# Optimization experiments

Measured on AMD Instinct MI355X. Metric: run time of the kernel, lower is better.

The kernel has to match this reference:

```python
import jax, jax.numpy as jnp
import numpy as np

DIM = 128
N = 16          # num_nodes
B = 8           # batch size
H = 4096        # MLP hidden width
SLOPE = 0.01    # LeakyReLU default negative slope
PI_ITERS = 50   # fixed-iteration power iteration (max_error=1e-5 regime)


def setup_inputs() -> dict:
    key = jax.random.key(0)
    ks = jax.random.split(key, 12)
    w = lambda k, shape: jax.random.normal(k, shape, jnp.float32) * 0.02
    return {
        "nodes_embeddings": jax.random.normal(ks[0], (B, N, DIM), jnp.float32),
        "graphs_embeddings": jax.random.normal(ks[1], (B, DIM), jnp.float32),
        "Ts": jax.random.uniform(ks[2], (B, N, N), jnp.float32),
        "W1": w(ks[3], (2 * DIM, H)), "b1": jnp.zeros((H,), jnp.float32),
        "W2": w(ks[4], (H, H)),       "b2": jnp.zeros((H,), jnp.float32),
        "W3": w(ks[5], (H, H)),       "b3": jnp.zeros((H,), jnp.float32),
        "W4": w(ks[6], (H, N * N)),   "b4": jnp.zeros((N * N,), jnp.float32),
    }


def _mlp(x, W1, b1, W2, b2, W3, b3, W4, b4):
    # Linear -> LeakyReLU -> (Dropout=eval identity), x3, then Linear -> LeakyReLU -> Sigmoid
    h = jax.nn.leaky_relu(x @ W1 + b1, SLOPE)
    h = jax.nn.leaky_relu(h @ W2 + b2, SLOPE)
    h = jax.nn.leaky_relu(h @ W3 + b3, SLOPE)
    return jax.nn.sigmoid(jax.nn.leaky_relu(h @ W4 + b4, SLOPE))


def _power_iteration(A):
    # A: (..., n, n), entries > 0 (sigmoid outputs) -> dominant (Perron) eigenvector.
    v0 = jnp.ones(A.shape[:-1], A.dtype)
    def step(v, _):
        w = jnp.einsum('...ij,...j->...i', A, v)
        v = w / jnp.linalg.norm(w, axis=-1, keepdims=True)
        return v, None
    v, _ = jax.lax.scan(step, v0, None, length=PI_ITERS)
    return v


def reference(nodes_embeddings, graphs_embeddings, Ts, W1, b1, W2, b2, W3, b3, W4, b4):
    Bn, Nn, D = nodes_embeddings.shape
    P = Nn * Nn
    pair = jnp.arange(P)
    s_ids = pair // Nn  # outer loop index s
    t_ids = pair % Nn   # inner loop index t

    embT = jnp.transpose(nodes_embeddings, (1, 0, 2))      # (N, B, D)
    s_all = embT[s_ids]                                    # (P, B, D)
    t_all = embT[t_ids]                                    # (P, B, D)
    # Faithful to torch.stack([s, t]).view(batch, 2*dim): a flat reinterpretation,
    # NOT a per-row concat. stack axis=1 -> (P, 2, B, D) then reshape -> (P, B, 2D).
    x = jnp.stack([s_all, t_all], axis=1).reshape(P, Bn, 2 * D)

    pol = _mlp(x.reshape(P * Bn, 2 * D), W1, b1, W2, b2, W3, b3, W4, b4)
    pol = pol.reshape(P, Bn, Nn, Nn)                       # predecessor prob matrices

    vec = _power_iteration(pol)                            # (P, B, N)
    v_src = vec[pair, :, s_ids]                            # (P, B) eigenvector[src]
    T_pair = jnp.transpose(Ts.reshape(Bn, P), (1, 0))      # (P, B), pair order s*N+t

    contrib = vec / v_src[:, :, None] * T_pair[:, :, None]  # (P, B, N)
    return jnp.sum(contrib, axis=0)                         # (B, N) == Cs
```

## Files before the change

### kernel.cpp

```cpp
#include <hip/hip_runtime.h>

typedef unsigned short u16;
typedef unsigned int u32;
typedef __attribute__((ext_vector_type(8))) short short8;
typedef __attribute__((ext_vector_type(4))) float f32x4;

__device__ __forceinline__ u16 f2bf(float f) {
    unsigned u = __float_as_uint(f);
    return (u16)((u + 0x7FFFu + ((u >> 16) & 1u)) >> 16);
}
__device__ __forceinline__ u32 pack2(float a, float b) {
    return ((u32)f2bf(b) << 16) | (u32)f2bf(a);
}

#define ROR1 0x121
#define ROR2 0x122
#define ROR4 0x124
#define ROR8 0x128
template<int C> __device__ __forceinline__ float dppf(float x) {
    int i = __float_as_int(x);
    return __int_as_float(__builtin_amdgcn_update_dpp(i, i, C, 0xF, 0xF, false));
}
template<int C> __device__ __forceinline__ int dppi(int x) {
    return __builtin_amdgcn_update_dpp(x, x, C, 0xF, 0xF, false);
}

__device__ __forceinline__ void stage_w(const float* __restrict__ W, int N,
                                        int krow0, int c0, int wv, int lane,
                                        u16 (*Wlds)[136])
{
    int cb = wv * 8;
    const float* s0 = W + (size_t)(krow0 + 2 * lane) * N + c0 + cb;
    float4 r0a = ((const float4*)s0)[0];
    float4 r0b = ((const float4*)s0)[1];
    const float* s1 = s0 + N;
    float4 r1a = ((const float4*)s1)[0];
    float4 r1b = ((const float4*)s1)[1];
    u32* wb = (u32*)&Wlds[0][0];
    wb[(cb + 0) * 68 + lane] = pack2(r0a.x, r1a.x);
    wb[(cb + 1) * 68 + lane] = pack2(r0a.y, r1a.y);
    wb[(cb + 2) * 68 + lane] = pack2(r0a.z, r1a.z);
    wb[(cb + 3) * 68 + lane] = pack2(r0a.w, r1a.w);
    wb[(cb + 4) * 68 + lane] = pack2(r0b.x, r1b.x);
    wb[(cb + 5) * 68 + lane] = pack2(r0b.y, r1b.y);
    wb[(cb + 6) * 68 + lane] = pack2(r0b.z, r1b.z);
    wb[(cb + 7) * 68 + lane] = pack2(r0b.w, r1b.w);
}

__global__ __launch_bounds__(256) void k_gemm(
    const u16* __restrict__ A,
    const float* __restrict__ W,
    float* __restrict__ Cp,
    int K, int N, int kchunk)
{
    __shared__ __align__(16) u16 Alds[64][136];
    __shared__ __align__(16) u16 Wlds[32][136];
    int tid = threadIdx.x;
    int wv = tid >> 6, lane = tid & 63, c = lane & 15, g = lane >> 4;
    int c0 = blockIdx.x * 32;
    int k0 = blockIdx.y * kchunk;
    f32x4 acc0 = {0.f,0.f,0.f,0.f}, acc1 = {0.f,0.f,0.f,0.f};

    for (int kc = 0; kc < kchunk; kc += 128) {
        {
            int row = tid >> 2, seg = tid & 3;
            const uint4* src = (const uint4*)(A + (size_t)row * K + k0 + kc + seg * 32);
            uint4* dst = (uint4*)&Alds[row][seg * 32];
            dst[0] = src[0]; dst[1] = src[1]; dst[2] = src[2]; dst[3] = src[3];
        }
        stage_w(W, N, k0 + kc, c0, wv, lane, Wlds);
        __syncthreads();
        #pragma unroll
        for (int ks = 0; ks < 4; ++ks) {
            int kk = ks * 32 + g * 8;
            short8 a8 = *(const short8*)&Alds[wv * 16 + c][kk];
            short8 b0 = *(const short8*)&Wlds[c][kk];
            short8 b1 = *(const short8*)&Wlds[16 + c][kk];
            acc0 = __builtin_amdgcn_mfma_f32_16x16x32_bf16(a8, b0, acc0, 0, 0, 0);
            acc1 = __builtin_amdgcn_mfma_f32_16x16x32_bf16(a8, b1, acc1, 0, 0, 0);
        }
        __syncthreads();
    }
    float* out = Cp + (size_t)blockIdx.y * 64 * N;
    int rbase = wv * 16 + g * 4;
    #pragma unroll
    for (int rr = 0; rr < 4; ++rr) {
        out[(size_t)(rbase + rr) * N + c0 + c]      = acc0[rr];
        out[(size_t)(rbase + rr) * N + c0 + 16 + c] = acc1[rr];
    }
}

__global__ __launch_bounds__(256) void k_gemm_l1(
    const float* __restrict__ emb,
    const float* __restrict__ W,
    float* __restrict__ Cp)
{
    __shared__ __align__(16) u16 Alds[64][136];
    __shared__ __align__(16) u16 Wlds[32][136];
    int tid = threadIdx.x;
    int wv = tid >> 6, lane = tid & 63, c = lane & 15, g = lane >> 4;
    int c0 = blockIdx.x * 32;
    int half = blockIdx.y;
    f32x4 acc0 = {0.f,0.f,0.f,0.f}, acc1 = {0.f,0.f,0.f,0.f};

    {
        int row = tid >> 2, seg = tid & 3;
        int b = 2 * (row & 3) + half, nd = row >> 2;
        const float4* src = (const float4*)(emb + (b * 16 + nd) * 128 + seg * 32);
        u32* dst = (u32*)&Alds[row][seg * 32];
        #pragma unroll
        for (int t = 0; t < 8; ++t) {
            float4 f = src[t];
            dst[2 * t]     = pack2(f.x, f.y);
            dst[2 * t + 1] = pack2(f.z, f.w);
        }
    }
    stage_w(W, 4096, half * 128, c0, wv, lane, Wlds);
    __syncthreads();
    #pragma unroll
    for (int ks = 0; ks < 4; ++ks) {
        int kk = ks * 32 + g * 8;
        short8 a8 = *(const short8*)&Alds[wv * 16 + c][kk];
        short8 b0 = *(const short8*)&Wlds[c][kk];
        short8 b1 = *(const short8*)&Wlds[16 + c][kk];
        acc0 = __builtin_amdgcn_mfma_f32_16x16x32_bf16(a8, b0, acc0, 0, 0, 0);
        acc1 = __builtin_amdgcn_mfma_f32_16x16x32_bf16(a8, b1, acc1, 0, 0, 0);
    }
    float* out = Cp + (size_t)half * 64 * 4096;
    int rbase = wv * 16 + g * 4;
    #pragma unroll
    for (int rr = 0; rr < 4; ++rr) {
        out[(size_t)(rbase + rr) * 4096 + c0 + c]      = acc0[rr];
        out[(size_t)(rbase + rr) * 4096 + c0 + 16 + c] = acc1[rr];
    }
}

__global__ void k_reduce(const float* __restrict__ Cp, const float* __restrict__ bias,
                         u16* __restrict__ Hb, float* __restrict__ Pf,
                         int N, int ksplit, int mode)
{
    int idx = blockIdx.x * 256 + threadIdx.x;
    int col = idx & (N - 1);
    float s = bias[col];
    for (int k = 0; k < ksplit; ++k) s += Cp[(size_t)k * 64 * N + idx];
    float a = (s >= 0.f) ? s : 0.01f * s;
    if (mode == 0) Hb[idx] = f2bf(a);
    else           Pf[idx] = 1.0f / (1.0f + __expf(-a));
}

__global__ __launch_bounds__(1024) void k_power_out(
    const float* __restrict__ pol,
    const float* __restrict__ Ts,
    float* __restrict__ out)
{
    __shared__ float pol_lds[16384];
    __shared__ float w_lds[64][16];
    __shared__ float Ts_lds[2048];
    __shared__ float Cmat[8][16];

    int tid = threadIdx.x;
    int m = tid >> 4, r = tid & 15;

    {
        const float4* p4 = (const float4*)(pol + tid * 16);
        float4* q4 = (float4*)&pol_lds[tid * 16];
        q4[0] = p4[0]; q4[1] = p4[1]; q4[2] = p4[2]; q4[3] = p4[3];
    }
    Ts_lds[tid] = Ts[tid];
    Ts_lds[tid + 1024] = Ts[tid + 1024];
    __syncthreads();

    float Mr[8], Ms[8];
    {
        int mb = m * 256 + r * 16;
        int idx = r;
        #pragma unroll
        for (int k = 0; k < 8; ++k) { Mr[k] = pol_lds[mb + idx]; idx = dppi<ROR1>(idx); }
        #pragma unroll
        for (int k = 0; k < 8; ++k) { Ms[k] = pol_lds[mb + idx]; idx = dppi<ROR1>(idx); }
    }

    float v = 1.0f;
    #pragma unroll 1
    for (int it = 0; it < 50; ++it) {
        float va = v, vb = dppf<ROR8>(v);
        float w = 0.f, w2 = 0.f;
        #pragma unroll
        for (int k = 0; k < 8; ++k) {
            w  = fmaf(Mr[k], va, w);
            w2 = fmaf(Ms[k], vb, w2);
            if (k < 7) { va = dppf<ROR1>(va); vb = dppf<ROR1>(vb); }
        }
        w += w2;
        if ((it & 7) == 7) {
            float s = w;
            s += dppf<ROR8>(s); s += dppf<ROR4>(s);
            s += dppf<ROR2>(s); s += dppf<ROR1>(s);
            w *= 1.0f / s;
        }
        v = w;
    }
    w_lds[m][r] = v;
    __syncthreads();

    if (tid < 128) {
        int b = tid >> 4, x = tid & 15;
        float s = 0.f;
        if (b < 4) {
            const float* row = &Ts_lds[(b * 16 + x) * 16];
            #pragma unroll
            for (int t = 0; t < 16; ++t) s += row[t];
        } else {
            int j = b - 4;
            #pragma unroll
            for (int si = 0; si < 16; ++si)
                s += Ts_lds[(b * 16 + si) * 16 + x] / w_lds[x * 4 + j][si];
        }
        Cmat[b][x] = s;
    }
    __syncthreads();

    if (tid < 128) {
        int b = tid >> 4, n = tid & 15;
        float o = 0.f;
        if (b < 4) {
            #pragma unroll
            for (int si = 0; si < 16; ++si) {
                const float* wr = w_lds[si * 4 + b];
                o += wr[n] / wr[si] * Cmat[b][si];
            }
        } else {
            int j = b - 4;
            #pragma unroll
            for (int t = 0; t < 16; ++t)
                o += w_lds[t * 4 + j][n] * Cmat[b][t];
        }
        out[b * 16 + n] = o;
    }
}

extern "C" void kernel_launch(void* const* d_in, const int* in_sizes, int n_in,
                              void* d_out, int out_size, void* d_ws, size_t ws_size,
                              hipStream_t stream)
{
    const float* emb = (const float*)d_in[0];
    const float* Ts  = (const float*)d_in[2];
    const float* W1  = (const float*)d_in[3];  const float* b1 = (const float*)d_in[4];
    const float* W2  = (const float*)d_in[5];  const float* b2 = (const float*)d_in[6];
    const float* W3  = (const float*)d_in[7];  const float* b3 = (const float*)d_in[8];
    const float* W4  = (const float*)d_in[9];  const float* b4 = (const float*)d_in[10];
    float* outp = (float*)d_out;

    char* ws = (char*)d_ws;
    u16*   Ha  = (u16*)(ws + 0);
    u16*   Hb  = (u16*)(ws + 524288);
    float* pol = (float*)(ws + 1048576);
    float* Cp  = (float*)(ws + 1114112);

    int KS = 16;
    while (KS > 2 && (size_t)1114112 + (size_t)KS * 1048576 > ws_size) KS >>= 1;
    int kchunk = 4096 / KS;

    k_gemm_l1<<<dim3(128, 2), 256, 0, stream>>>(emb, W1, Cp);
    k_reduce<<<1024, 256, 0, stream>>>(Cp, b1, Ha, nullptr, 4096, 2, 0);

    k_gemm<<<dim3(128, KS), 256, 0, stream>>>(Ha, W2, Cp, 4096, 4096, kchunk);
    k_reduce<<<1024, 256, 0, stream>>>(Cp, b2, Hb, nullptr, 4096, KS, 0);

    k_gemm<<<dim3(128, KS), 256, 0, stream>>>(Hb, W3, Cp, 4096, 4096, kchunk);
    k_reduce<<<1024, 256, 0, stream>>>(Cp, b3, Ha, nullptr, 4096, KS, 0);

    k_gemm<<<dim3(8, 32), 256, 0, stream>>>(Ha, W4, Cp, 4096, 256, 128);
    k_reduce<<<64, 256, 0, stream>>>(Cp, b4, nullptr, pol, 256, 32, 1);

    k_power_out<<<1, 1024, 0, stream>>>(pol, Ts, outp);

    (void)in_sizes; (void)n_in; (void)out_size; (void)ws_size;
}
```

Measured before the change: 94.26 us.

## Fuse whole MLP and power iteration into one cooperative persistent kernel

Replaces the chain of nine kernel launches with one cooperative kernel of 1024 blocks that uses grid-wide syncs between stages: the layer-1 GEMM, split-K GEMMs, reductions, the final sigmoid, a power iteration spread over four blocks, and the output combine. The GEMM inner loop also gains register prefetch of the next A/W chunk, and the split-K factor for the large layers drops from 16 to 8. The aim is to remove launch gaps and stage tails. The cost is grid.sync overhead and the need for all blocks to be co-resident, with a fallback to the separate launches if that is not possible.

```diff
diff --git a/kernel.cpp b/kernel.cpp
--- a/kernel.cpp
+++ b/kernel.cpp
@@ -1,4 +1,7 @@
 #include <hip/hip_runtime.h>
+#include <hip/hip_cooperative_groups.h>
+
+namespace cg = cooperative_groups;
 
 typedef unsigned short u16;
 typedef unsigned int u32;
@@ -25,51 +28,50 @@
     return __builtin_amdgcn_update_dpp(x, x, C, 0xF, 0xF, false);
 }
 
-__device__ __forceinline__ void stage_w(const float* __restrict__ W, int N,
-                                        int krow0, int c0, int wv, int lane,
-                                        u16 (*Wlds)[136])
-{
+__device__ __forceinline__ void gemm_slice(
+    const u16* __restrict__ A, const float* __restrict__ W,
+    float* __restrict__ outC, int K, int N, int c0, int k0, int nchunk,
+    u16 (*Alds)[136], u16 (*Wlds)[136], int tid)
+{
+    int wv = tid >> 6, lane = tid & 63, c = lane & 15, g = lane >> 4;
+    int arow = tid >> 2, aseg = tid & 3;
     int cb = wv * 8;
-    const float* s0 = W + (size_t)(krow0 + 2 * lane) * N + c0 + cb;
-    float4 r0a = ((const float4*)s0)[0];
-    float4 r0b = ((const float4*)s0)[1];
-    const float* s1 = s0 + N;
-    float4 r1a = ((const float4*)s1)[0];
-    float4 r1b = ((const float4*)s1)[1];
-    u32* wb = (u32*)&Wlds[0][0];
-    wb[(cb + 0) * 68 + lane] = pack2(r0a.x, r1a.x);
-    wb[(cb + 1) * 68 + lane] = pack2(r0a.y, r1a.y);
-    wb[(cb + 2) * 68 + lane] = pack2(r0a.z, r1a.z);
-    wb[(cb + 3) * 68 + lane] = pack2(r0a.w, r1a.w);
-    wb[(cb + 4) * 68 + lane] = pack2(r0b.x, r1b.x);
-    wb[(cb + 5) * 68 + lane] = pack2(r0b.y, r1b.y);
-    wb[(cb + 6) * 68 + lane] = pack2(r0b.z, r1b.z);
-    wb[(cb + 7) * 68 + lane] = pack2(r0b.w, r1b.w);
-}
-
-__global__ __launch_bounds__(256) void k_gemm(
-    const u16* __restrict__ A,
-    const float* __restrict__ W,
-    float* __restrict__ Cp,
-    int K, int N, int kchunk)
-{
-    __shared__ __align__(16) u16 Alds[64][136];
-    __shared__ __align__(16) u16 Wlds[32][136];
-    int tid = threadIdx.x;
-    int wv = tid >> 6, lane = tid & 63, c = lane & 15, g = lane >> 4;
-    int c0 = blockIdx.x * 32;
-    int k0 = blockIdx.y * kchunk;
     f32x4 acc0 = {0.f,0.f,0.f,0.f}, acc1 = {0.f,0.f,0.f,0.f};
 
-    for (int kc = 0; kc < kchunk; kc += 128) {
+    uint4 ar0, ar1, ar2, ar3;
+    float4 w0, w1, w2, w3;
+    {
+        const uint4* asrc = (const uint4*)(A + (size_t)arow * K + k0 + aseg * 32);
+        ar0 = asrc[0]; ar1 = asrc[1]; ar2 = asrc[2]; ar3 = asrc[3];
+        const float* s0 = W + (size_t)(k0 + 2 * lane) * N + c0 + cb;
+        w0 = ((const float4*)s0)[0]; w1 = ((const float4*)s0)[1];
+        const float* s1 = s0 + N;
+        w2 = ((const float4*)s1)[0]; w3 = ((const float4*)s1)[1];
+    }
+    for (int ch = 0; ch < nchunk; ++ch) {
         {
-            int row = tid >> 2, seg = tid & 3;
-            const uint4* src = (const uint4*)(A + (size_t)row * K + k0 + kc + seg * 32);
-            uint4* dst = (uint4*)&Alds[row][seg * 32];
-            dst[0] = src[0]; dst[1] = src[1]; dst[2] = src[2]; dst[3] = src[3];
-        }
-        stage_w(W, N, k0 + kc, c0, wv, lane, Wlds);
-        __syncthreads();
+            uint4* dst = (uint4*)&Alds[arow][aseg * 32];
+            dst[0] = ar0; dst[1] = ar1; dst[2] = ar2; dst[3] = ar3;
+            u32* wb = (u32*)&Wlds[0][0];
+            wb[(cb + 0) * 68 + lane] = pack2(w0.x, w2.x);
+            wb[(cb + 1) * 68 + lane] = pack2(w0.y, w2.y);
+            wb[(cb + 2) * 68 + lane] = pack2(w0.z, w2.z);
+            wb[(cb + 3) * 68 + lane] = pack2(w0.w, w2.w);
+            wb[(cb + 4) * 68 + lane] = pack2(w1.x, w3.x);
+            wb[(cb + 5) * 68 + lane] = pack2(w1.y, w3.y);
+            wb[(cb + 6) * 68 + lane] = pack2(w1.z, w3.z);
+            wb[(cb + 7) * 68 + lane] = pack2(w1.w, w3.w);
+        }
+        __syncthreads();
+        if (ch + 1 < nchunk) {
+            int kn = k0 + (ch + 1) * 128;
+            const uint4* asrc = (const uint4*)(A + (size_t)arow * K + kn + aseg * 32);
+            ar0 = asrc[0]; ar1 = asrc[1]; ar2 = asrc[2]; ar3 = asrc[3];
+            const float* s0 = W + (size_t)(kn + 2 * lane) * N + c0 + cb;
+            w0 = ((const float4*)s0)[0]; w1 = ((const float4*)s0)[1];
+            const float* s1 = s0 + N;
+            w2 = ((const float4*)s1)[0]; w3 = ((const float4*)s1)[1];
+        }
         #pragma unroll
         for (int ks = 0; ks < 4; ++ks) {
             int kk = ks * 32 + g * 8;
@@ -81,18 +83,241 @@
         }
         __syncthreads();
     }
-    float* out = Cp + (size_t)blockIdx.y * 64 * N;
     int rbase = wv * 16 + g * 4;
     #pragma unroll
     for (int rr = 0; rr < 4; ++rr) {
-        out[(size_t)(rbase + rr) * N + c0 + c]      = acc0[rr];
-        out[(size_t)(rbase + rr) * N + c0 + 16 + c] = acc1[rr];
-    }
+        outC[(size_t)(rbase + rr) * N + c0 + c]      = acc0[rr];
+        outC[(size_t)(rbase + rr) * N + c0 + 16 + c] = acc1[rr];
+    }
+}
+
+struct MegaP {
+    const float *emb, *Ts, *W1, *b1, *W2, *b2, *W3, *b3, *W4, *b4;
+    float* out;
+    u16 *Ha, *Hb;
+    float *Cp, *wvec;
+};
+
+__global__ __launch_bounds__(256) void mega(MegaP p)
+{
+    __shared__ __align__(16) u16 Alds[64][136];
+    __shared__ __align__(16) u16 Wlds[32][136];
+    cg::grid_group grid = cg::this_grid();
+    int bid = blockIdx.x, tid = threadIdx.x;
+    int wv = tid >> 6, lane = tid & 63, c = lane & 15, g = lane >> 4;
+
+    if (bid < 256) {
+        int c0 = (bid & 127) * 32, half = bid >> 7;
+        {
+            int row = tid >> 2, seg = tid & 3;
+            int b = 2 * (row & 3) + half, nd = row >> 2;
+            const float4* src = (const float4*)(p.emb + (b * 16 + nd) * 128 + seg * 32);
+            u32* dst = (u32*)&Alds[row][seg * 32];
+            #pragma unroll
+            for (int t = 0; t < 8; ++t) {
+                float4 f = src[t];
+                dst[2 * t]     = pack2(f.x, f.y);
+                dst[2 * t + 1] = pack2(f.z, f.w);
+            }
+        }
+        {
+            int cb = wv * 8;
+            const float* s0 = p.W1 + (size_t)(half * 128 + 2 * lane) * 4096 + c0 + cb;
+            float4 r0a = ((const float4*)s0)[0], r0b = ((const float4*)s0)[1];
+            const float* s1 = s0 + 4096;
+            float4 r1a = ((const float4*)s1)[0], r1b = ((const float4*)s1)[1];
+            u32* wb = (u32*)&Wlds[0][0];
+            wb[(cb + 0) * 68 + lane] = pack2(r0a.x, r1a.x);
+            wb[(cb + 1) * 68 + lane] = pack2(r0a.y, r1a.y);
+            wb[(cb + 2) * 68 + lane] = pack2(r0a.z, r1a.z);
+            wb[(cb + 3) * 68 + lane] = pack2(r0a.w, r1a.w);
+            wb[(cb + 4) * 68 + lane] = pack2(r0b.x, r1b.x);
+            wb[(cb + 5) * 68 + lane] = pack2(r0b.y, r1b.y);
+            wb[(cb + 6) * 68 + lane] = pack2(r0b.z, r1b.z);
+            wb[(cb + 7) * 68 + lane] = pack2(r0b.w, r1b.w);
+        }
+        __syncthreads();
+        f32x4 acc0 = {0.f,0.f,0.f,0.f}, acc1 = {0.f,0.f,0.f,0.f};
+        #pragma unroll
+        for (int ks = 0; ks < 4; ++ks) {
+            int kk = ks * 32 + g * 8;
+            short8 a8 = *(const short8*)&Alds[wv * 16 + c][kk];
+            short8 b0 = *(const short8*)&Wlds[c][kk];
+            short8 b1 = *(const short8*)&Wlds[16 + c][kk];
+            acc0 = __builtin_amdgcn_mfma_f32_16x16x32_bf16(a8, b0, acc0, 0, 0, 0);
+            acc1 = __builtin_amdgcn_mfma_f32_16x16x32_bf16(a8, b1, acc1, 0, 0, 0);
+        }
+        float* out = p.Cp + (size_t)half * 262144;
+        int rbase = wv * 16 + g * 4;
+        #pragma unroll
+        for (int rr = 0; rr < 4; ++rr) {
+            out[(size_t)(rbase + rr) * 4096 + c0 + c]      = acc0[rr];
+            out[(size_t)(rbase + rr) * 4096 + c0 + 16 + c] = acc1[rr];
+        }
+        __syncthreads();
+    }
+    grid.sync();
+
+    {
+        int idx = bid * 256 + tid;
+        int col = idx & 4095;
+        float s = p.b1[col] + p.Cp[idx] + p.Cp[262144 + idx];
+        s = (s >= 0.f) ? s : 0.01f * s;
+        p.Ha[idx] = f2bf(s);
+    }
+    grid.sync();
+
+    gemm_slice(p.Ha, p.W2, p.Cp + (size_t)(bid >> 7) * 262144,
+               4096, 4096, (bid & 127) * 32, (bid >> 7) * 512, 4, Alds, Wlds, tid);
+    grid.sync();
+
+    {
+        int idx = bid * 256 + tid;
+        int col = idx & 4095;
+        float s = p.b2[col];
+        #pragma unroll
+        for (int k = 0; k < 8; ++k) s += p.Cp[(size_t)k * 262144 + idx];
+        s = (s >= 0.f) ? s : 0.01f * s;
+        p.Hb[idx] = f2bf(s);
+    }
+    grid.sync();
+
+    gemm_slice(p.Hb, p.W3, p.Cp + (size_t)(bid >> 7) * 262144,
+               4096, 4096, (bid & 127) * 32, (bid >> 7) * 512, 4, Alds, Wlds, tid);
+    grid.sync();
+
+    {
+        int idx = bid * 256 + tid;
+        int col = idx & 4095;
+        float s = p.b3[col];
+        #pragma unroll
+        for (int k = 0; k < 8; ++k) s += p.Cp[(size_t)k * 262144 + idx];
+        s = (s >= 0.f) ? s : 0.01f * s;
+        p.Ha[idx] = f2bf(s);
+    }
+    grid.sync();
+
+    if (bid < 256)
+        gemm_slice(p.Ha, p.W4, p.Cp + (size_t)(bid >> 3) * 16384,
+                   4096, 256, (bid & 7) * 32, (bid >> 3) * 128, 1, Alds, Wlds, tid);
+    grid.sync();
+
+    if (bid < 4) {
+        float* pol_lds = (float*)&Alds[0][0];
+        {
+            int lr = tid >> 4;
+            int gr = (bid << 4) + lr;
+            int cb4 = (tid & 15) << 4;
+            float accv[16];
+            #pragma unroll
+            for (int j = 0; j < 16; ++j) accv[j] = p.b4[cb4 + j];
+            for (int k = 0; k < 32; ++k) {
+                const float4* q = (const float4*)(p.Cp + (size_t)k * 16384 + gr * 256 + cb4);
+                #pragma unroll
+                for (int j = 0; j < 4; ++j) {
+                    float4 v = q[j];
+                    accv[4*j+0] += v.x; accv[4*j+1] += v.y;
+                    accv[4*j+2] += v.z; accv[4*j+3] += v.w;
+                }
+            }
+            #pragma unroll
+            for (int j = 0; j < 16; ++j) {
+                float a = accv[j];
+                a = (a >= 0.f) ? a : 0.01f * a;
+                pol_lds[lr * 256 + cb4 + j] = 1.0f / (1.0f + __expf(-a));
+            }
+        }
+        __syncthreads();
+        float Mr[8], Ms[8];
+        {
+            int mb = (tid >> 4) * 256 + (tid & 15) * 16;
+            int idx = tid & 15;
+            #pragma unroll
+            for (int k = 0; k < 8; ++k) { Mr[k] = pol_lds[mb + idx]; idx = dppi<ROR1>(idx); }
+            #pragma unroll
+            for (int k = 0; k < 8; ++k) { Ms[k] = pol_lds[mb + idx]; idx = dppi<ROR1>(idx); }
+        }
+        float v = 1.0f;
+        #pragma unroll 1
+        for (int it = 0; it < 50; ++it) {
+            float va = v, vb = dppf<ROR8>(v);
+            float w = 0.f, w2 = 0.f;
+            #pragma unroll
+            for (int k = 0; k < 8; ++k) {
+                w  = fmaf(Mr[k], va, w);
+                w2 = fmaf(Ms[k], vb, w2);
+                if (k < 7) { va = dppf<ROR1>(va); vb = dppf<ROR1>(vb); }
+            }
+            w += w2;
+            if ((it & 7) == 7) {
+                float s = w;
+                s += dppf<ROR8>(s); s += dppf<ROR4>(s);
+                s += dppf<ROR2>(s); s += dppf<ROR1>(s);
+                w *= 1.0f / s;
+            }
+            v = w;
+        }
+        p.wvec[((bid << 4) + (tid >> 4)) * 16 + (tid & 15)] = v;
+        __syncthreads();
+    }
+    grid.sync();
+
+    if (bid == 0) {
+        float* w_lds  = (float*)&Alds[0][0];
+        float* Ts_lds = (float*)&Wlds[0][0];
+        float* Cmat   = Ts_lds + 2048;
+        ((float4*)w_lds)[tid]        = ((const float4*)p.wvec)[tid];
+        ((float4*)Ts_lds)[tid]       = ((const float4*)p.Ts)[tid];
+        ((float4*)Ts_lds)[256 + tid] = ((const float4*)p.Ts)[256 + tid];
+        __syncthreads();
+        if (tid < 128) {
+            int b = tid >> 4, x = tid & 15;
+            float s = 0.f;
+            if (b < 4) {
+                #pragma unroll
+                for (int t = 0; t < 16; ++t) s += Ts_lds[(b * 16 + x) * 16 + t];
+            } else {
+                int j = b - 4;
+                #pragma unroll
+                for (int si = 0; si < 16; ++si)
+                    s += Ts_lds[(b * 16 + si) * 16 + x] / w_lds[(x * 4 + j) * 16 + si];
+            }
+            Cmat[b * 16 + x] = s;
+        }
+        __syncthreads();
+        if (tid < 128) {
+            int b = tid >> 4, n = tid & 15;
+            float o = 0.f;
+            if (b < 4) {
+                #pragma unroll
+                for (int si = 0; si < 16; ++si) {
+                    const float* wr = &w_lds[(si * 4 + b) * 16];
+                    o += wr[n] / wr[si] * Cmat[b * 16 + si];
+                }
+            } else {
+                int j = b - 4;
+                #pragma unroll
+                for (int t = 0; t < 16; ++t)
+                    o += w_lds[(t * 4 + j) * 16 + n] * Cmat[b * 16 + t];
+            }
+            p.out[b * 16 + n] = o;
+        }
+    }
+}
+
+__global__ __launch_bounds__(256) void k_gemm(
+    const u16* __restrict__ A, const float* __restrict__ W,
+    float* __restrict__ Cp, int K, int N, int kchunk)
+{
+    __shared__ __align__(16) u16 Alds[64][136];
+    __shared__ __align__(16) u16 Wlds[32][136];
+    int tid = threadIdx.x;
+    gemm_slice(A, W, Cp + (size_t)blockIdx.y * 64 * N, K, N,
+               blockIdx.x * 32, blockIdx.y * kchunk, kchunk / 128, Alds, Wlds, tid);
 }
 
 __global__ __launch_bounds__(256) void k_gemm_l1(
-    const float* __restrict__ emb,
-    const float* __restrict__ W,
+    const float* __restrict__ emb, const float* __restrict__ W,
     float* __restrict__ Cp)
 {
     __shared__ __align__(16) u16 Alds[64][136];
@@ -101,8 +326,6 @@
     int wv = tid >> 6, lane = tid & 63, c = lane & 15, g = lane >> 4;
     int c0 = blockIdx.x * 32;
     int half = blockIdx.y;
-    f32x4 acc0 = {0.f,0.f,0.f,0.f}, acc1 = {0.f,0.f,0.f,0.f};
-
     {
         int row = tid >> 2, seg = tid & 3;
         int b = 2 * (row & 3) + half, nd = row >> 2;
@@ -115,8 +338,24 @@
             dst[2 * t + 1] = pack2(f.z, f.w);
         }
     }
-    stage_w(W, 4096, half * 128, c0, wv, lane, Wlds);
+    {
+        int cb = wv * 8;
+        const float* s0 = W + (size_t)(half * 128 + 2 * lane) * 4096 + c0 + cb;
+        float4 r0a = ((const float4*)s0)[0], r0b = ((const float4*)s0)[1];
+        const float* s1 = s0 + 4096;
+        float4 r1a = ((const float4*)s1)[0], r1b = ((const float4*)s1)[1];
+        u32* wb = (u32*)&Wlds[0][0];
+        wb[(cb + 0) * 68 + lane] = pack2(r0a.x, r1a.x);
+        wb[(cb + 1) * 68 + lane] = pack2(r0a.y, r1a.y);
+        wb[(cb + 2) * 68 + lane] = pack2(r0a.z, r1a.z);
+        wb[(cb + 3) * 68 + lane] = pack2(r0a.w, r1a.w);
+        wb[(cb + 4) * 68 + lane] = pack2(r0b.x, r1b.x);
+        wb[(cb + 5) * 68 + lane] = pack2(r0b.y, r1b.y);
+        wb[(cb + 6) * 68 + lane] = pack2(r0b.z, r1b.z);
+        wb[(cb + 7) * 68 + lane] = pack2(r0b.w, r1b.w);
+    }
     __syncthreads();
+    f32x4 acc0 = {0.f,0.f,0.f,0.f}, acc1 = {0.f,0.f,0.f,0.f};
     #pragma unroll
     for (int ks = 0; ks < 4; ++ks) {
         int kk = ks * 32 + g * 8;
@@ -149,18 +388,15 @@
 }
 
 __global__ __launch_bounds__(1024) void k_power_out(
-    const float* __restrict__ pol,
-    const float* __restrict__ Ts,
+    const float* __restrict__ pol, const float* __restrict__ Ts,
     float* __restrict__ out)
 {
     __shared__ float pol_lds[16384];
     __shared__ float w_lds[64][16];
     __shared__ float Ts_lds[2048];
     __shared__ float Cmat[8][16];
-
     int tid = threadIdx.x;
     int m = tid >> 4, r = tid & 15;
-
     {
         const float4* p4 = (const float4*)(pol + tid * 16);
         float4* q4 = (float4*)&pol_lds[tid * 16];
@@ -169,7 +405,6 @@
     Ts_lds[tid] = Ts[tid];
     Ts_lds[tid + 1024] = Ts[tid + 1024];
     __syncthreads();
-
     float Mr[8], Ms[8];
     {
         int mb = m * 256 + r * 16;
@@ -179,7 +414,6 @@
         #pragma unroll
         for (int k = 0; k < 8; ++k) { Ms[k] = pol_lds[mb + idx]; idx = dppi<ROR1>(idx); }
     }
-
     float v = 1.0f;
     #pragma unroll 1
     for (int it = 0; it < 50; ++it) {
@@ -202,14 +436,12 @@
     }
     w_lds[m][r] = v;
     __syncthreads();
-
     if (tid < 128) {
         int b = tid >> 4, x = tid & 15;
         float s = 0.f;
         if (b < 4) {
-            const float* row = &Ts_lds[(b * 16 + x) * 16];
-            #pragma unroll
-            for (int t = 0; t < 16; ++t) s += row[t];
+            #pragma unroll
+            for (int t = 0; t < 16; ++t) s += Ts_lds[(b * 16 + x) * 16 + t];
         } else {
             int j = b - 4;
             #pragma unroll
@@ -219,7 +451,6 @@
         Cmat[b][x] = s;
     }
     __syncthreads();
-
     if (tid < 128) {
         int b = tid >> 4, n = tid & 15;
         float o = 0.f;
@@ -252,28 +483,34 @@
     float* outp = (float*)d_out;
 
     char* ws = (char*)d_ws;
-    u16*   Ha  = (u16*)(ws + 0);
-    u16*   Hb  = (u16*)(ws + 524288);
-    float* pol = (float*)(ws + 1048576);
-    float* Cp  = (float*)(ws + 1114112);
-
-    int KS = 16;
-    while (KS > 2 && (size_t)1114112 + (size_t)KS * 1048576 > ws_size) KS >>= 1;
-    int kchunk = 4096 / KS;
-
-    k_gemm_l1<<<dim3(128, 2), 256, 0, stream>>>(emb, W1, Cp);
-    k_reduce<<<1024, 256, 0, stream>>>(Cp, b1, Ha, nullptr, 4096, 2, 0);
-
-    k_gemm<<<dim3(128, KS), 256, 0, stream>>>(Ha, W2, Cp, 4096, 4096, kchunk);
-    k_reduce<<<1024, 256, 0, stream>>>(Cp, b2, Hb, nullptr, 4096, KS, 0);
-
-    k_gemm<<<dim3(128, KS), 256, 0, stream>>>(Hb, W3, Cp, 4096, 4096, kchunk);
-    k_reduce<<<1024, 256, 0, stream>>>(Cp, b3, Ha, nullptr, 4096, KS, 0);
-
-    k_gemm<<<dim3(8, 32), 256, 0, stream>>>(Ha, W4, Cp, 4096, 256, 128);
-    k_reduce<<<64, 256, 0, stream>>>(Cp, b4, nullptr, pol, 256, 32, 1);
-
-    k_power_out<<<1, 1024, 0, stream>>>(pol, Ts, outp);
+    u16*   Ha   = (u16*)(ws + 0);
+    u16*   Hb   = (u16*)(ws + 524288);
+    float* Cp   = (float*)(ws + 1048576);
+    float* wvec = (float*)(ws + 9437184);
+    float* pol  = (float*)(ws + 9441280);
+
+    MegaP prm { emb, Ts, W1, b1, W2, b2, W3, b3, W4, b4, outp, Ha, Hb, Cp, wvec };
+
+    int nb = 0;
+    hipError_t qe = hipOccupancyMaxActiveBlocksPerMultiprocessor(&nb, (const void*)mega, 256, 0);
+    bool coop = (qe == hipSuccess && nb >= 4);
+    if (coop) {
+        void* args[] = { &prm };
+        hipError_t le = hipLaunchCooperativeKernel((const void*)mega, dim3(1024), dim3(256),
+                                                   args, 0, stream);
+        if (le != hipSuccess) coop = false;
+    }
+    if (!coop) {
+        k_gemm_l1<<<dim3(128, 2), 256, 0, stream>>>(emb, W1, Cp);
+        k_reduce<<<1024, 256, 0, stream>>>(Cp, b1, Ha, nullptr, 4096, 2, 0);
+        k_gemm<<<dim3(128, 8), 256, 0, stream>>>(Ha, W2, Cp, 4096, 4096, 512);
+        k_reduce<<<1024, 256, 0, stream>>>(Cp, b2, Hb, nullptr, 4096, 8, 0);
+        k_gemm<<<dim3(128, 8), 256, 0, stream>>>(Hb, W3, Cp, 4096, 4096, 512);
+        k_reduce<<<1024, 256, 0, stream>>>(Cp, b3, Ha, nullptr, 4096, 8, 0);
+        k_gemm<<<dim3(8, 32), 256, 0, stream>>>(Ha, W4, Cp, 4096, 256, 128);
+        k_reduce<<<64, 256, 0, stream>>>(Cp, b4, nullptr, pol, 256, 32, 1);
+        k_power_out<<<1, 1024, 0, stream>>>(pol, Ts, outp);
+    }
 
     (void)in_sizes; (void)n_in; (void)out_size; (void)ws_size;
 }
```

After: 85.73 us. -9.0%, faster.

## Fuse split-K reduction and bias/activation into GEMMs with in-block K-split and prefetch

Applied to the files above, without the earlier changes.

Removes the separate k_reduce kernels and the fp32 partial-sum buffer. Each GEMM block now runs four 256-thread K-groups that split K inside the block, prefetch the next chunk into registers, reduce partial sums through LDS, and apply bias, LeakyReLU and bf16 or sigmoid output directly. This cuts kernel launches and the global traffic of writing and reading partials. In exchange the large layers use only 128 blocks (8 for the last) instead of 128×16, so there is much less parallelism across the GPU for the weight streaming.

```diff
diff --git a/kernel.cpp b/kernel.cpp
--- a/kernel.cpp
+++ b/kernel.cpp
@@ -25,50 +25,48 @@
     return __builtin_amdgcn_update_dpp(x, x, C, 0xF, 0xF, false);
 }
 
-__device__ __forceinline__ void stage_w(const float* __restrict__ W, int N,
-                                        int krow0, int c0, int wv, int lane,
-                                        u16 (*Wlds)[136])
-{
-    int cb = wv * 8;
-    const float* s0 = W + (size_t)(krow0 + 2 * lane) * N + c0 + cb;
-    float4 r0a = ((const float4*)s0)[0];
-    float4 r0b = ((const float4*)s0)[1];
-    const float* s1 = s0 + N;
-    float4 r1a = ((const float4*)s1)[0];
-    float4 r1b = ((const float4*)s1)[1];
-    u32* wb = (u32*)&Wlds[0][0];
-    wb[(cb + 0) * 68 + lane] = pack2(r0a.x, r1a.x);
-    wb[(cb + 1) * 68 + lane] = pack2(r0a.y, r1a.y);
-    wb[(cb + 2) * 68 + lane] = pack2(r0a.z, r1a.z);
-    wb[(cb + 3) * 68 + lane] = pack2(r0a.w, r1a.w);
-    wb[(cb + 4) * 68 + lane] = pack2(r0b.x, r1b.x);
-    wb[(cb + 5) * 68 + lane] = pack2(r0b.y, r1b.y);
-    wb[(cb + 6) * 68 + lane] = pack2(r0b.z, r1b.z);
-    wb[(cb + 7) * 68 + lane] = pack2(r0b.w, r1b.w);
-}
-
-__global__ __launch_bounds__(256) void k_gemm(
-    const u16* __restrict__ A,
+__global__ __launch_bounds__(256) void k_l1(
+    const float* __restrict__ emb,
     const float* __restrict__ W,
-    float* __restrict__ Cp,
-    int K, int N, int kchunk)
+    const float* __restrict__ bias,
+    u16* __restrict__ H)
 {
     __shared__ __align__(16) u16 Alds[64][136];
     __shared__ __align__(16) u16 Wlds[32][136];
     int tid = threadIdx.x;
     int wv = tid >> 6, lane = tid & 63, c = lane & 15, g = lane >> 4;
     int c0 = blockIdx.x * 32;
-    int k0 = blockIdx.y * kchunk;
+    int cb = wv * 8;
     f32x4 acc0 = {0.f,0.f,0.f,0.f}, acc1 = {0.f,0.f,0.f,0.f};
 
-    for (int kc = 0; kc < kchunk; kc += 128) {
+    for (int ch = 0; ch < 2; ++ch) {
         {
             int row = tid >> 2, seg = tid & 3;
-            const uint4* src = (const uint4*)(A + (size_t)row * K + k0 + kc + seg * 32);
-            uint4* dst = (uint4*)&Alds[row][seg * 32];
-            dst[0] = src[0]; dst[1] = src[1]; dst[2] = src[2]; dst[3] = src[3];
-        }
-        stage_w(W, N, k0 + kc, c0, wv, lane, Wlds);
+            int b = 2 * (row & 3) + ch, nd = row >> 2;
+            const float4* src = (const float4*)(emb + (b * 16 + nd) * 128 + seg * 32);
+            u32* dst = (u32*)&Alds[row][seg * 32];
+            #pragma unroll
+            for (int q = 0; q < 8; ++q) {
+                float4 f = src[q];
+                dst[2 * q]     = pack2(f.x, f.y);
+                dst[2 * q + 1] = pack2(f.z, f.w);
+            }
+        }
+        {
+            const float* s0 = W + (size_t)(ch * 128 + 2 * lane) * 4096 + c0 + cb;
+            float4 p0 = ((const float4*)s0)[0], p1 = ((const float4*)s0)[1];
+            const float* s1 = s0 + 4096;
+            float4 p2 = ((const float4*)s1)[0], p3 = ((const float4*)s1)[1];
+            u32* wb = (u32*)&Wlds[0][0];
+            wb[(cb + 0) * 68 + lane] = pack2(p0.x, p2.x);
+            wb[(cb + 1) * 68 + lane] = pack2(p0.y, p2.y);
+            wb[(cb + 2) * 68 + lane] = pack2(p0.z, p2.z);
+            wb[(cb + 3) * 68 + lane] = pack2(p0.w, p2.w);
+            wb[(cb + 4) * 68 + lane] = pack2(p1.x, p3.x);
+            wb[(cb + 5) * 68 + lane] = pack2(p1.y, p3.y);
+            wb[(cb + 6) * 68 + lane] = pack2(p1.z, p3.z);
+            wb[(cb + 7) * 68 + lane] = pack2(p1.w, p3.w);
+        }
         __syncthreads();
         #pragma unroll
         for (int ks = 0; ks < 4; ++ks) {
@@ -81,71 +79,115 @@
         }
         __syncthreads();
     }
-    float* out = Cp + (size_t)blockIdx.y * 64 * N;
     int rbase = wv * 16 + g * 4;
     #pragma unroll
     for (int rr = 0; rr < 4; ++rr) {
-        out[(size_t)(rbase + rr) * N + c0 + c]      = acc0[rr];
-        out[(size_t)(rbase + rr) * N + c0 + 16 + c] = acc1[rr];
-    }
-}
-
-__global__ __launch_bounds__(256) void k_gemm_l1(
-    const float* __restrict__ emb,
+        int col0 = c0 + c, col1 = c0 + 16 + c;
+        float v0 = acc0[rr] + bias[col0]; v0 = (v0 >= 0.f) ? v0 : 0.01f * v0;
+        float v1 = acc1[rr] + bias[col1]; v1 = (v1 >= 0.f) ? v1 : 0.01f * v1;
+        H[(size_t)(rbase + rr) * 4096 + col0] = f2bf(v0);
+        H[(size_t)(rbase + rr) * 4096 + col1] = f2bf(v1);
+    }
+}
+
+template<int MODE>
+__global__ __launch_bounds__(1024) void k_mid(
+    const u16* __restrict__ A,
     const float* __restrict__ W,
-    float* __restrict__ Cp)
+    const float* __restrict__ bias,
+    u16* __restrict__ Hb,
+    float* __restrict__ Pf,
+    int N)
 {
-    __shared__ __align__(16) u16 Alds[64][136];
-    __shared__ __align__(16) u16 Wlds[32][136];
+    __shared__ __align__(16) u16 Alds[4][64][136];
+    __shared__ __align__(16) u16 Wlds[4][32][136];
     int tid = threadIdx.x;
-    int wv = tid >> 6, lane = tid & 63, c = lane & 15, g = lane >> 4;
+    int kg = tid >> 8;
+    int t  = tid & 255;
+    int wv = t >> 6, lane = t & 63, c = lane & 15, g = lane >> 4;
     int c0 = blockIdx.x * 32;
-    int half = blockIdx.y;
+    int arow = t >> 2, aseg = t & 3;
+    int cb = wv * 8;
     f32x4 acc0 = {0.f,0.f,0.f,0.f}, acc1 = {0.f,0.f,0.f,0.f};
 
+    uint4 a0, a1, a2, a3;
+    float4 q0, q1, q2, q3;
     {
-        int row = tid >> 2, seg = tid & 3;
-        int b = 2 * (row & 3) + half, nd = row >> 2;
-        const float4* src = (const float4*)(emb + (b * 16 + nd) * 128 + seg * 32);
-        u32* dst = (u32*)&Alds[row][seg * 32];
-        #pragma unroll
-        for (int t = 0; t < 8; ++t) {
-            float4 f = src[t];
-            dst[2 * t]     = pack2(f.x, f.y);
-            dst[2 * t + 1] = pack2(f.z, f.w);
-        }
-    }
-    stage_w(W, 4096, half * 128, c0, wv, lane, Wlds);
+        const uint4* as = (const uint4*)(A + ((size_t)arow << 12) + kg * 128 + aseg * 32);
+        a0 = as[0]; a1 = as[1]; a2 = as[2]; a3 = as[3];
+        const float* s0 = W + (size_t)(kg * 128 + 2 * lane) * N + c0 + cb;
+        q0 = ((const float4*)s0)[0]; q1 = ((const float4*)s0)[1];
+        const float* s1 = s0 + N;
+        q2 = ((const float4*)s1)[0]; q3 = ((const float4*)s1)[1];
+    }
+    for (int it = 0; it < 8; ++it) {
+        {
+            uint4* ad = (uint4*)&Alds[kg][arow][aseg * 32];
+            ad[0] = a0; ad[1] = a1; ad[2] = a2; ad[3] = a3;
+            u32* wb = (u32*)&Wlds[kg][0][0];
+            wb[(cb + 0) * 68 + lane] = pack2(q0.x, q2.x);
+            wb[(cb + 1) * 68 + lane] = pack2(q0.y, q2.y);
+            wb[(cb + 2) * 68 + lane] = pack2(q0.z, q2.z);
+            wb[(cb + 3) * 68 + lane] = pack2(q0.w, q2.w);
+            wb[(cb + 4) * 68 + lane] = pack2(q1.x, q3.x);
+            wb[(cb + 5) * 68 + lane] = pack2(q1.y, q3.y);
+            wb[(cb + 6) * 68 + lane] = pack2(q1.z, q3.z);
+            wb[(cb + 7) * 68 + lane] = pack2(q1.w, q3.w);
+        }
+        __syncthreads();
+        if (it < 7) {
+            int ch = (it + 1) * 4 + kg;
+            const uint4* as = (const uint4*)(A + ((size_t)arow << 12) + ch * 128 + aseg * 32);
+            a0 = as[0]; a1 = as[1]; a2 = as[2]; a3 = as[3];
+            const float* s0 = W + (size_t)(ch * 128 + 2 * lane) * N + c0 + cb;
+            q0 = ((const float4*)s0)[0]; q1 = ((const float4*)s0)[1];
+            const float* s1 = s0 + N;
+            q2 = ((const float4*)s1)[0]; q3 = ((const float4*)s1)[1];
+        }
+        #pragma unroll
+        for (int ks = 0; ks < 4; ++ks) {
+            int kk = ks * 32 + g * 8;
+            short8 a8 = *(const short8*)&Alds[kg][wv * 16 + c][kk];
+            short8 b0 = *(const short8*)&Wlds[kg][c][kk];
+            short8 b1 = *(const short8*)&Wlds[kg][16 + c][kk];
+            acc0 = __builtin_amdgcn_mfma_f32_16x16x32_bf16(a8, b0, acc0, 0, 0, 0);
+            acc1 = __builtin_amdgcn_mfma_f32_16x16x32_bf16(a8, b1, acc1, 0, 0, 0);
+        }
+        __syncthreads();
+    }
+
+    float* scr = (float*)&Alds[0][0][0];
+    if (kg > 0) {
+        float4* s4 = (float4*)&scr[((kg - 1) * 256 + t) * 8];
+        s4[0] = *(float4*)&acc0;
+        s4[1] = *(float4*)&acc1;
+    }
     __syncthreads();
-    #pragma unroll
-    for (int ks = 0; ks < 4; ++ks) {
-        int kk = ks * 32 + g * 8;
-        short8 a8 = *(const short8*)&Alds[wv * 16 + c][kk];
-        short8 b0 = *(const short8*)&Wlds[c][kk];
-        short8 b1 = *(const short8*)&Wlds[16 + c][kk];
-        acc0 = __builtin_amdgcn_mfma_f32_16x16x32_bf16(a8, b0, acc0, 0, 0, 0);
-        acc1 = __builtin_amdgcn_mfma_f32_16x16x32_bf16(a8, b1, acc1, 0, 0, 0);
-    }
-    float* out = Cp + (size_t)half * 64 * 4096;
-    int rbase = wv * 16 + g * 4;
-    #pragma unroll
-    for (int rr = 0; rr < 4; ++rr) {
-        out[(size_t)(rbase + rr) * 4096 + c0 + c]      = acc0[rr];
-        out[(size_t)(rbase + rr) * 4096 + c0 + 16 + c] = acc1[rr];
-    }
-}
-
-__global__ void k_reduce(const float* __restrict__ Cp, const float* __restrict__ bias,
-                         u16* __restrict__ Hb, float* __restrict__ Pf,
-                         int N, int ksplit, int mode)
-{
-    int idx = blockIdx.x * 256 + threadIdx.x;
-    int col = idx & (N - 1);
-    float s = bias[col];
-    for (int k = 0; k < ksplit; ++k) s += Cp[(size_t)k * 64 * N + idx];
-    float a = (s >= 0.f) ? s : 0.01f * s;
-    if (mode == 0) Hb[idx] = f2bf(a);
-    else           Pf[idx] = 1.0f / (1.0f + __expf(-a));
+    if (kg == 0) {
+        #pragma unroll
+        for (int q = 0; q < 3; ++q) {
+            const float4* s4 = (const float4*)&scr[(q * 256 + t) * 8];
+            float4 p0 = s4[0], p1 = s4[1];
+            acc0[0] += p0.x; acc0[1] += p0.y; acc0[2] += p0.z; acc0[3] += p0.w;
+            acc1[0] += p1.x; acc1[1] += p1.y; acc1[2] += p1.z; acc1[3] += p1.w;
+        }
+        int rbase = wv * 16 + g * 4;
+        #pragma unroll
+        for (int rr = 0; rr < 4; ++rr) {
+            int col0 = c0 + c, col1 = c0 + 16 + c;
+            float v0 = acc0[rr] + bias[col0];
+            float v1 = acc1[rr] + bias[col1];
+            v0 = (v0 >= 0.f) ? v0 : 0.01f * v0;
+            v1 = (v1 >= 0.f) ? v1 : 0.01f * v1;
+            if (MODE == 0) {
+                Hb[(size_t)(rbase + rr) * N + col0] = f2bf(v0);
+                Hb[(size_t)(rbase + rr) * N + col1] = f2bf(v1);
+            } else {
+                Pf[(size_t)(rbase + rr) * N + col0] = 1.0f / (1.0f + __expf(-v0));
+                Pf[(size_t)(rbase + rr) * N + col1] = 1.0f / (1.0f + __expf(-v1));
+            }
+        }
+    }
 }
 
 __global__ __launch_bounds__(1024) void k_power_out(
@@ -255,25 +297,12 @@
     u16*   Ha  = (u16*)(ws + 0);
     u16*   Hb  = (u16*)(ws + 524288);
     float* pol = (float*)(ws + 1048576);
-    float* Cp  = (float*)(ws + 1114112);
-
-    int KS = 16;
-    while (KS > 2 && (size_t)1114112 + (size_t)KS * 1048576 > ws_size) KS >>= 1;
-    int kchunk = 4096 / KS;
-
-    k_gemm_l1<<<dim3(128, 2), 256, 0, stream>>>(emb, W1, Cp);
-    k_reduce<<<1024, 256, 0, stream>>>(Cp, b1, Ha, nullptr, 4096, 2, 0);
-
-    k_gemm<<<dim3(128, KS), 256, 0, stream>>>(Ha, W2, Cp, 4096, 4096, kchunk);
-    k_reduce<<<1024, 256, 0, stream>>>(Cp, b2, Hb, nullptr, 4096, KS, 0);
-
-    k_gemm<<<dim3(128, KS), 256, 0, stream>>>(Hb, W3, Cp, 4096, 4096, kchunk);
-    k_reduce<<<1024, 256, 0, stream>>>(Cp, b3, Ha, nullptr, 4096, KS, 0);
-
-    k_gemm<<<dim3(8, 32), 256, 0, stream>>>(Ha, W4, Cp, 4096, 256, 128);
-    k_reduce<<<64, 256, 0, stream>>>(Cp, b4, nullptr, pol, 256, 32, 1);
-
-    k_power_out<<<1, 1024, 0, stream>>>(pol, Ts, outp);
+
+    k_l1      <<<128, 256,  0, stream>>>(emb, W1, b1, Ha);
+    k_mid<0>  <<<128, 1024, 0, stream>>>(Ha, W2, b2, Hb, nullptr, 4096);
+    k_mid<0>  <<<128, 1024, 0, stream>>>(Hb, W3, b3, Ha, nullptr, 4096);
+    k_mid<1>  <<<8,   1024, 0, stream>>>(Ha, W4, b4, nullptr, pol, 256);
+    k_power_out<<<1,  1024, 0, stream>>>(pol, Ts, outp);
 
     (void)in_sizes; (void)n_in; (void)out_size; (void)ws_size;
 }
```

Result: slower. 129.7 us (+37.6%).

## Widen GEMM tiles to 128 columns with register-prefetched K pipeline and fused L1 epilogue

Applied to the files above, without the earlier changes.

Replaces the 32-column, 128-deep GEMM tile with a 128-column tile stepping 32 along K, and prefetches the next A and W slices into registers while the current slice is computed. Layer 1 folds bias, LeakyReLU and the bf16 cast into the GEMM epilogue, so it no longer needs a separate reduce pass. The split-K factor for the large layers drops from 16 to 8, which shrinks the partial-sum traffic. The cost is a much smaller grid (256 blocks for the big layers, 32 for layer 1), which risks leaving many CUs idle. Launch bounds also force one block per SM.

```diff
diff --git a/kernel.cpp b/kernel.cpp
--- a/kernel.cpp
+++ b/kernel.cpp
@@ -25,113 +25,109 @@
     return __builtin_amdgcn_update_dpp(x, x, C, 0xF, 0xF, false);
 }
 
-__device__ __forceinline__ void stage_w(const float* __restrict__ W, int N,
-                                        int krow0, int c0, int wv, int lane,
-                                        u16 (*Wlds)[136])
-{
-    int cb = wv * 8;
-    const float* s0 = W + (size_t)(krow0 + 2 * lane) * N + c0 + cb;
-    float4 r0a = ((const float4*)s0)[0];
-    float4 r0b = ((const float4*)s0)[1];
-    const float* s1 = s0 + N;
-    float4 r1a = ((const float4*)s1)[0];
-    float4 r1b = ((const float4*)s1)[1];
-    u32* wb = (u32*)&Wlds[0][0];
-    wb[(cb + 0) * 68 + lane] = pack2(r0a.x, r1a.x);
-    wb[(cb + 1) * 68 + lane] = pack2(r0a.y, r1a.y);
-    wb[(cb + 2) * 68 + lane] = pack2(r0a.z, r1a.z);
-    wb[(cb + 3) * 68 + lane] = pack2(r0a.w, r1a.w);
-    wb[(cb + 4) * 68 + lane] = pack2(r0b.x, r1b.x);
-    wb[(cb + 5) * 68 + lane] = pack2(r0b.y, r1b.y);
-    wb[(cb + 6) * 68 + lane] = pack2(r0b.z, r1b.z);
-    wb[(cb + 7) * 68 + lane] = pack2(r0b.w, r1b.w);
-}
-
-__global__ __launch_bounds__(256) void k_gemm(
-    const u16* __restrict__ A,
-    const float* __restrict__ W,
-    float* __restrict__ Cp,
-    int K, int N, int kchunk)
-{
-    __shared__ __align__(16) u16 Alds[64][136];
-    __shared__ __align__(16) u16 Wlds[32][136];
+template<int SRC, int EPI>
+__global__ __launch_bounds__(256, 1) void k_gemm(
+    const u16* __restrict__ A, const float* __restrict__ emb,
+    const float* __restrict__ W, const float* __restrict__ bias,
+    float* __restrict__ Cp, u16* __restrict__ Ho, float* __restrict__ Po,
+    int N, int kchunk)
+{
+    __shared__ __align__(16) u16 Alds[64][40];
+    __shared__ __align__(16) u32 Wlds[16 * 132];
     int tid = threadIdx.x;
     int wv = tid >> 6, lane = tid & 63, c = lane & 15, g = lane >> 4;
-    int c0 = blockIdx.x * 32;
+    int c0 = blockIdx.x * 128;
     int k0 = blockIdx.y * kchunk;
-    f32x4 acc0 = {0.f,0.f,0.f,0.f}, acc1 = {0.f,0.f,0.f,0.f};
-
-    for (int kc = 0; kc < kchunk; kc += 128) {
+    int nit = kchunk >> 5;
+
+    int ar = tid >> 2, aseg = tid & 3;
+    int kp = tid >> 4, cbase = (tid & 15) * 8;
+
+    f32x4 acc[8];
+    #pragma unroll
+    for (int n = 0; n < 8; ++n) acc[n] = (f32x4){0.f, 0.f, 0.f, 0.f};
+
+    uint4 av;
+    float4 q0, q1, q2, q3;
+
+    {
+        if (SRC == 0) {
+            av = *(const uint4*)(A + (size_t)ar * 4096 + k0 + aseg * 8);
+        } else {
+            int e0 = aseg * 8;
+            int b = 2 * (ar & 3) + (e0 >> 7), d = e0 & 127;
+            const float4* s = (const float4*)(emb + (b * 16 + (ar >> 2)) * 128 + d);
+            float4 f0 = s[0], f1 = s[1];
+            av.x = pack2(f0.x, f0.y); av.y = pack2(f0.z, f0.w);
+            av.z = pack2(f1.x, f1.y); av.w = pack2(f1.z, f1.w);
+        }
+        const float* s0 = W + (size_t)(k0 + 2 * kp) * N + c0 + cbase;
+        q0 = ((const float4*)s0)[0]; q1 = ((const float4*)s0)[1];
+        const float* s1 = s0 + N;
+        q2 = ((const float4*)s1)[0]; q3 = ((const float4*)s1)[1];
+    }
+
+    for (int it = 0; it < nit; ++it) {
+        *(uint4*)&Alds[ar][aseg * 8] = av;
         {
-            int row = tid >> 2, seg = tid & 3;
-            const uint4* src = (const uint4*)(A + (size_t)row * K + k0 + kc + seg * 32);
-            uint4* dst = (uint4*)&Alds[row][seg * 32];
-            dst[0] = src[0]; dst[1] = src[1]; dst[2] = src[2]; dst[3] = src[3];
-        }
-        stage_w(W, N, k0 + kc, c0, wv, lane, Wlds);
+            uint4 w0, w1;
+            w0.x = pack2(q0.x, q2.x); w0.y = pack2(q0.y, q2.y);
+            w0.z = pack2(q0.z, q2.z); w0.w = pack2(q0.w, q2.w);
+            w1.x = pack2(q1.x, q3.x); w1.y = pack2(q1.y, q3.y);
+            w1.z = pack2(q1.z, q3.z); w1.w = pack2(q1.w, q3.w);
+            uint4* wd = (uint4*)&Wlds[kp * 132 + cbase];
+            wd[0] = w0; wd[1] = w1;
+        }
         __syncthreads();
-        #pragma unroll
-        for (int ks = 0; ks < 4; ++ks) {
-            int kk = ks * 32 + g * 8;
-            short8 a8 = *(const short8*)&Alds[wv * 16 + c][kk];
-            short8 b0 = *(const short8*)&Wlds[c][kk];
-            short8 b1 = *(const short8*)&Wlds[16 + c][kk];
-            acc0 = __builtin_amdgcn_mfma_f32_16x16x32_bf16(a8, b0, acc0, 0, 0, 0);
-            acc1 = __builtin_amdgcn_mfma_f32_16x16x32_bf16(a8, b1, acc1, 0, 0, 0);
+
+        if (it + 1 < nit) {
+            int kc = (it + 1) * 32;
+            if (SRC == 0) {
+                av = *(const uint4*)(A + (size_t)ar * 4096 + k0 + kc + aseg * 8);
+            } else {
+                int e0 = kc + aseg * 8;
+                int b = 2 * (ar & 3) + (e0 >> 7), d = e0 & 127;
+                const float4* s = (const float4*)(emb + (b * 16 + (ar >> 2)) * 128 + d);
+                float4 f0 = s[0], f1 = s[1];
+                av.x = pack2(f0.x, f0.y); av.y = pack2(f0.z, f0.w);
+                av.z = pack2(f1.x, f1.y); av.w = pack2(f1.z, f1.w);
+            }
+            const float* s0 = W + (size_t)(k0 + kc + 2 * kp) * N + c0 + cbase;
+            q0 = ((const float4*)s0)[0]; q1 = ((const float4*)s0)[1];
+            const float* s1 = s0 + N;
+            q2 = ((const float4*)s1)[0]; q3 = ((const float4*)s1)[1];
+        }
+
+        short8 a8 = *(const short8*)&Alds[wv * 16 + c][g * 8];
+        #pragma unroll
+        for (int n = 0; n < 8; ++n) {
+            int base = n * 16 + c;
+            union { u32 u[4]; short8 s; } bb;
+            bb.u[0] = Wlds[(g * 4 + 0) * 132 + base];
+            bb.u[1] = Wlds[(g * 4 + 1) * 132 + base];
+            bb.u[2] = Wlds[(g * 4 + 2) * 132 + base];
+            bb.u[3] = Wlds[(g * 4 + 3) * 132 + base];
+            acc[n] = __builtin_amdgcn_mfma_f32_16x16x32_bf16(a8, bb.s, acc[n], 0, 0, 0);
         }
         __syncthreads();
     }
-    float* out = Cp + (size_t)blockIdx.y * 64 * N;
-    int rbase = wv * 16 + g * 4;
+
     #pragma unroll
-    for (int rr = 0; rr < 4; ++rr) {
-        out[(size_t)(rbase + rr) * N + c0 + c]      = acc0[rr];
-        out[(size_t)(rbase + rr) * N + c0 + 16 + c] = acc1[rr];
-    }
-}
-
-__global__ __launch_bounds__(256) void k_gemm_l1(
-    const float* __restrict__ emb,
-    const float* __restrict__ W,
-    float* __restrict__ Cp)
-{
-    __shared__ __align__(16) u16 Alds[64][136];
-    __shared__ __align__(16) u16 Wlds[32][136];
-    int tid = threadIdx.x;
-    int wv = tid >> 6, lane = tid & 63, c = lane & 15, g = lane >> 4;
-    int c0 = blockIdx.x * 32;
-    int half = blockIdx.y;
-    f32x4 acc0 = {0.f,0.f,0.f,0.f}, acc1 = {0.f,0.f,0.f,0.f};
-
-    {
-        int row = tid >> 2, seg = tid & 3;
-        int b = 2 * (row & 3) + half, nd = row >> 2;
-        const float4* src = (const float4*)(emb + (b * 16 + nd) * 128 + seg * 32);
-        u32* dst = (u32*)&Alds[row][seg * 32];
-        #pragma unroll
-        for (int t = 0; t < 8; ++t) {
-            float4 f = src[t];
-            dst[2 * t]     = pack2(f.x, f.y);
-            dst[2 * t + 1] = pack2(f.z, f.w);
-        }
-    }
-    stage_w(W, 4096, half * 128, c0, wv, lane, Wlds);
-    __syncthreads();
-    #pragma unroll
-    for (int ks = 0; ks < 4; ++ks) {
-        int kk = ks * 32 + g * 8;
-        short8 a8 = *(const short8*)&Alds[wv * 16 + c][kk];
-        short8 b0 = *(const short8*)&Wlds[c][kk];
-        short8 b1 = *(const short8*)&Wlds[16 + c][kk];
-        acc0 = __builtin_amdgcn_mfma_f32_16x16x32_bf16(a8, b0, acc0, 0, 0, 0);
-        acc1 = __builtin_amdgcn_mfma_f32_16x16x32_bf16(a8, b1, acc1, 0, 0, 0);
-    }
-    float* out = Cp + (size_t)half * 64 * 4096;
-    int rbase = wv * 16 + g * 4;
-    #pragma unroll
-    for (int rr = 0; rr < 4; ++rr) {
-        out[(size_t)(rbase + rr) * 4096 + c0 + c]      = acc0[rr];
-        out[(size_t)(rbase + rr) * 4096 + c0 + 16 + c] = acc1[rr];
+    for (int n = 0; n < 8; ++n) {
+        #pragma unroll
+        for (int rr = 0; rr < 4; ++rr) {
+            int grow = wv * 16 + g * 4 + rr;
+            int gcol = c0 + n * 16 + c;
+            float v = acc[n][rr];
+            if (EPI == 0) {
+                Cp[(size_t)blockIdx.y * 64 * N + (size_t)grow * N + gcol] = v;
+            } else {
+                v += bias[gcol];
+                v = (v >= 0.f) ? v : 0.01f * v;
+                if (EPI == 1) Ho[(size_t)grow * N + gcol] = f2bf(v);
+                else          Po[(size_t)grow * N + gcol] = 1.0f / (1.0f + __expf(-v));
+            }
+        }
     }
 }
 
@@ -257,20 +253,19 @@
     float* pol = (float*)(ws + 1048576);
     float* Cp  = (float*)(ws + 1114112);
 
-    int KS = 16;
-    while (KS > 2 && (size_t)1114112 + (size_t)KS * 1048576 > ws_size) KS >>= 1;
-    int kchunk = 4096 / KS;
-
-    k_gemm_l1<<<dim3(128, 2), 256, 0, stream>>>(emb, W1, Cp);
-    k_reduce<<<1024, 256, 0, stream>>>(Cp, b1, Ha, nullptr, 4096, 2, 0);
-
-    k_gemm<<<dim3(128, KS), 256, 0, stream>>>(Ha, W2, Cp, 4096, 4096, kchunk);
-    k_reduce<<<1024, 256, 0, stream>>>(Cp, b2, Hb, nullptr, 4096, KS, 0);
-
-    k_gemm<<<dim3(128, KS), 256, 0, stream>>>(Hb, W3, Cp, 4096, 4096, kchunk);
-    k_reduce<<<1024, 256, 0, stream>>>(Cp, b3, Ha, nullptr, 4096, KS, 0);
-
-    k_gemm<<<dim3(8, 32), 256, 0, stream>>>(Ha, W4, Cp, 4096, 256, 128);
+    k_gemm<1, 1><<<dim3(32, 1), 256, 0, stream>>>(
+        nullptr, emb, W1, b1, nullptr, Ha, nullptr, 4096, 256);
+
+    k_gemm<0, 0><<<dim3(32, 8), 256, 0, stream>>>(
+        Ha, nullptr, W2, nullptr, Cp, nullptr, nullptr, 4096, 512);
+    k_reduce<<<1024, 256, 0, stream>>>(Cp, b2, Hb, nullptr, 4096, 8, 0);
+
+    k_gemm<0, 0><<<dim3(32, 8), 256, 0, stream>>>(
+        Hb, nullptr, W3, nullptr, Cp, nullptr, nullptr, 4096, 512);
+    k_reduce<<<1024, 256, 0, stream>>>(Cp, b3, Ha, nullptr, 4096, 8, 0);
+
+    k_gemm<0, 0><<<dim3(2, 32), 256, 0, stream>>>(
+        Ha, nullptr, W4, nullptr, Cp, nullptr, nullptr, 256, 128);
     k_reduce<<<64, 256, 0, stream>>>(Cp, b4, nullptr, pol, 256, 32, 1);
 
     k_power_out<<<1, 1024, 0, stream>>>(pol, Ts, outp);
```

Measured after the change: 85.79 us. 9.0% less time.
